# Optimization experiments

Measured on AMD Instinct MI355X. Metric: run time of the kernel, lower is better.

Reference implementation:

```python
import jax, jax.numpy as jnp
import numpy as np

T_MAX = 0.5
LN_EPS = 1e-5
B, N, D = 256, 16384, 512
NNZ = N * 33  # ~ (2*top_k+1) nonzeros per row of the sparse Laplacian
DF = 4 * D
DT = 32  # time-embedding hidden size


def _layernorm(x, g, b):
    mu = jnp.mean(x, axis=-1, keepdims=True)
    var = jnp.mean((x - mu) ** 2, axis=-1, keepdims=True)
    return (x - mu) * jax.lax.rsqrt(var + LN_EPS) * g + b


def setup_inputs() -> dict:
    key = jax.random.key(0)
    ks = jax.random.split(key, 16)

    def lin_w(k, fan_out, fan_in):
        return jax.random.normal(k, (fan_out, fan_in), jnp.float32) * (1.0 / np.sqrt(fan_in))

    inp = {}
    inp["x0"] = jax.random.uniform(ks[0], (B, N), jnp.float32)
    inp["t"] = jax.random.uniform(ks[1], (B,), jnp.float32)
    inp["L_vals"] = jax.random.normal(ks[2], (NNZ,), jnp.float32) * 0.1
    inp["W_in"] = lin_w(ks[3], D, N)
    inp["b_in"] = jnp.zeros((D,), jnp.float32)
    inp["W_out"] = lin_w(ks[4], N, D)
    inp["b_out"] = jnp.zeros((N,), jnp.float32)
    inp["W_qkv"] = lin_w(ks[5], 3 * D, D)
    inp["b_qkv"] = jnp.zeros((3 * D,), jnp.float32)
    inp["W_o"] = lin_w(ks[6], D, D)
    inp["b_o"] = jnp.zeros((D,), jnp.float32)
    inp["g1"] = jnp.ones((D,), jnp.float32)
    inp["be1"] = jnp.zeros((D,), jnp.float32)
    inp["g2"] = jnp.ones((D,), jnp.float32)
    inp["be2"] = jnp.zeros((D,), jnp.float32)
    inp["W_f1"] = lin_w(ks[7], DF, D)
    inp["b_f1"] = jnp.zeros((DF,), jnp.float32)
    inp["W_f2"] = lin_w(ks[8], D, DF)
    inp["b_f2"] = jnp.zeros((D,), jnp.float32)
    inp["W_t1"] = lin_w(ks[9], DT, 1)
    inp["b_t1"] = jnp.zeros((DT,), jnp.float32)
    inp["W_t2"] = lin_w(ks[10], D, DT)
    inp["b_t2"] = jnp.zeros((D,), jnp.float32)
    inp["L_rows"] = jax.random.randint(ks[11], (NNZ,), 0, N, jnp.int32)
    inp["L_cols"] = jax.random.randint(ks[12], (NNZ,), 0, N, jnp.int32)
    return inp


def reference(x0, t, L_vals, W_in, b_in, W_out, b_out, W_qkv, b_qkv, W_o, b_o,
              g1, be1, g2, be2, W_f1, b_f1, W_f2, b_f2, W_t1, b_t1, W_t2, b_t2,
              L_rows, L_cols):
    n_items = x0.shape[1]
    d_model = W_in.shape[0]
    t_cont = t * T_MAX  # per-sample diffusion time (explicit input, not RNG)

    # Batched sparse Laplacian diffusion (replaces the per-row torch.sparse.mm loop):
    # (L @ x.T)[i, b] = sum_e L_vals[e] * x0[b, L_cols[e]] aggregated to row L_rows[e]
    contrib = x0[:, L_cols] * L_vals                                  # (B, NNZ)
    Lx = jax.ops.segment_sum(contrib.T, L_rows, num_segments=n_items)  # (N, B)
    x_t = x0 - t_cont[:, None] * Lx.T                                  # (B, N)

    # Denoiser (eval mode: dropout off)
    h = x_t @ W_in.T + b_in                                            # (B, D)
    t_norm = t_cont / T_MAX
    te = jax.nn.silu(t_norm[:, None] @ W_t1.T + b_t1) @ W_t2.T + b_t2  # (B, D)
    h = h + te

    # MultiheadAttention on a length-1 sequence: softmax over one key is exactly 1,
    # so attn_out = out_proj(V) with V = h @ W_v.T + b_v.
    qkv = h @ W_qkv.T + b_qkv                                          # (B, 3D)
    v = qkv[:, 2 * d_model:]
    attn_out = v @ W_o.T + b_o

    h = _layernorm(h + attn_out, g1, be1)
    ff = jax.nn.gelu(h @ W_f1.T + b_f1, approximate=False) @ W_f2.T + b_f2
    h = _layernorm(h + ff, g2, be2)

    pred = h @ W_out.T + b_out                                         # (B, N)
    return jnp.mean((pred - x0) ** 2)
```

## Files before the change

kernel.cpp:

```cpp
#include <hip/hip_runtime.h>
#include <math.h>

#define Bb   256
#define Nn   16384
#define Dd   512
#define NNZn 540672
#define DFf  2048
#define SLOT 128

#define BK_BLKS 528
#define TR_BLKS 1024
#define CVT_BLKS 2048
#define MG_BLKS 64
#define BV_BLKS 2
#define BK0 0
#define TR0 (BK0 + BK_BLKS)
#define CVT0 (TR0 + TR_BLKS)
#define MG0 (CVT0 + CVT_BLKS)
#define BV0 (MG0 + MG_BLKS)
#define PREP_BLKS (BV0 + BV_BLKS)

typedef __bf16 bf16;
typedef __bf16 bf16x4 __attribute__((ext_vector_type(4)));
typedef __bf16 bf16x8 __attribute__((ext_vector_type(8)));
typedef float  f32x4  __attribute__((ext_vector_type(4)));

__device__ __forceinline__ void gload16(const void* g, void* l) {
  __builtin_amdgcn_global_load_lds(
      (const __attribute__((address_space(1))) unsigned int*)g,
      (__attribute__((address_space(3))) unsigned int*)l, 16, 0, 0);
}

__global__ __launch_bounds__(256) void k_prep(
    const float* __restrict__ w_v, const float* __restrict__ w_o,
    const float* __restrict__ w_f1, const float* __restrict__ w_f2,
    bf16* __restrict__ o_f1, bf16* __restrict__ o_f2,
    bf16* __restrict__ w_ov,
    const float* __restrict__ b_o, const float* __restrict__ b_v,
    float* __restrict__ bsum,
    const float* __restrict__ x0, bf16* __restrict__ x0T,
    const int* __restrict__ rows, const int* __restrict__ cols,
    const float* __restrict__ vals,
    int* __restrict__ counts, int2* __restrict__ ents) {
  __shared__ __align__(16) char smem[16640];
  const int blk = blockIdx.x, tid = threadIdx.x;

  if (blk < TR0) {
    int i0 = blk * 1024 + tid;
    int r[4], c[4]; float v[4];
#pragma unroll
    for (int q = 0; q < 4; q++) {
      int i = i0 + q * 256;
      r[q] = rows[i]; c[q] = cols[i]; v[q] = vals[i];
    }
    int p[4];
#pragma unroll
    for (int q = 0; q < 4; q++) p[q] = atomicAdd(&counts[r[q]], 1);
#pragma unroll
    for (int q = 0; q < 4; q++)
      if (p[q] < SLOT)
        ents[(size_t)r[q] * SLOT + p[q]] = make_int2(c[q], __float_as_int(v[q]));
  } else if (blk < CVT0) {
    float (*tile)[65] = (float(*)[65])smem;
    int bx = blk - TR0;
    int n0 = (bx & 255) * 64, b0 = (bx >> 8) * 64;
    int tx = tid & 63, ty = tid >> 6;
#pragma unroll
    for (int i = 0; i < 16; i++) {
      int bl = ty * 16 + i;
      tile[bl][tx] = x0[(size_t)(b0 + bl) * Nn + n0 + tx];
    }
    __syncthreads();
#pragma unroll
    for (int i = 0; i < 16; i++) {
      int nl = ty * 16 + i;
      x0T[(size_t)(n0 + nl) * Bb + b0 + tx] = (bf16)tile[tx][nl];
    }
  } else if (blk < MG0) {
    int v4 = (blk - CVT0) * 256 + tid;
    const float* s; bf16* d; int base;
    if (v4 < 262144) { s = w_f1; d = o_f1; base = 0; }
    else             { s = w_f2; d = o_f2; base = 262144; }
    int idx = (v4 - base) * 4;
    float4 x = *(const float4*)(s + idx);
    bf16x4 o;
    o[0] = (bf16)x.x; o[1] = (bf16)x.y; o[2] = (bf16)x.z; o[3] = (bf16)x.w;
    *(bf16x4*)(d + idx) = o;
  } else if (blk < BV0) {
    bf16* As = (bf16*)smem;
    bf16* Bs = (bf16*)(smem + 4096);
    int mg = blk - MG0;
    int m0 = (mg >> 3) * 64, n0 = (mg & 7) * 64;
    const int lane = tid & 63, w = tid >> 6;
    const int wm = w >> 1, wn = w & 1;
    f32x4 acc[2][2];
#pragma unroll
    for (int i = 0; i < 2; i++)
#pragma unroll
      for (int j = 0; j < 2; j++) acc[i][j] = {0.f, 0.f, 0.f, 0.f};
    for (int e0 = 0; e0 < Dd; e0 += 32) {
      __syncthreads();
#pragma unroll
      for (int p = 0; p < 2; p++) {
        int u = p * 256 + tid;
        int row = u >> 3, sub = u & 7;
        float4 x = *(const float4*)(w_o + (size_t)(m0 + row) * Dd + e0 + sub * 4);
        bf16x4 o;
        o[0] = (bf16)x.x; o[1] = (bf16)x.y; o[2] = (bf16)x.z; o[3] = (bf16)x.w;
        *(bf16x4*)(As + row * 32 + sub * 4) = o;
      }
#pragma unroll
      for (int p = 0; p < 2; p++) {
        int u = p * 256 + tid;
        int el = u >> 4, jq = u & 15;
        float4 x = *(const float4*)(w_v + (size_t)(e0 + el) * Dd + n0 + jq * 4);
        Bs[(jq * 4 + 0) * 32 + el] = (bf16)x.x;
        Bs[(jq * 4 + 1) * 32 + el] = (bf16)x.y;
        Bs[(jq * 4 + 2) * 32 + el] = (bf16)x.z;
        Bs[(jq * 4 + 3) * 32 + el] = (bf16)x.w;
      }
      __syncthreads();
      bf16x8 af[2], bfr[2];
#pragma unroll
      for (int i = 0; i < 2; i++)
        af[i] = *(const bf16x8*)(As + (wm * 32 + i * 16 + (lane & 15)) * 32 + (lane >> 4) * 8);
#pragma unroll
      for (int j = 0; j < 2; j++)
        bfr[j] = *(const bf16x8*)(Bs + (wn * 32 + j * 16 + (lane & 15)) * 32 + (lane >> 4) * 8);
#pragma unroll
      for (int i = 0; i < 2; i++)
#pragma unroll
        for (int j = 0; j < 2; j++)
          acc[i][j] = __builtin_amdgcn_mfma_f32_16x16x32_bf16(af[i], bfr[j], acc[i][j], 0, 0, 0);
    }
#pragma unroll
    for (int i = 0; i < 2; i++)
#pragma unroll
      for (int j = 0; j < 2; j++) {
        int jj = n0 + wn * 32 + j * 16 + (lane & 15);
        int dB = m0 + wm * 32 + i * 16 + ((lane >> 4) << 2);
#pragma unroll
        for (int r = 0; r < 4; r++)
          w_ov[(size_t)(dB + r) * Dd + jj] = (bf16)acc[i][j][r];
      }
  } else {
    int d = (blk - BV0) * 256 + tid;
    float s = b_o[d];
    for (int e = 0; e < Dd; e += 4) {
      float4 wo = *(const float4*)(w_o + (size_t)d * Dd + e);
      float4 bv = *(const float4*)(b_v + e);
      s += wo.x * bv.x + wo.y * bv.y + wo.z * bv.z + wo.w * bv.w;
    }
    bsum[d] = s;
  }
}

__global__ __launch_bounds__(256) void k_lx(const bf16x4* __restrict__ x0T4,
                                            const int* __restrict__ counts,
                                            const int2* __restrict__ ents,
                                            bf16x4* __restrict__ Lx4) {
  int w = threadIdx.x >> 6, lane = threadIdx.x & 63;
  int r = blockIdx.x * 4 + w;
  __shared__ int2 esm[4][64];
  int cnt = counts[r];
  const int2* ep = ents + (size_t)r * SLOT;
  f32x4 a = {0.f, 0.f, 0.f, 0.f}, b = {0.f, 0.f, 0.f, 0.f};
  f32x4 c = {0.f, 0.f, 0.f, 0.f}, d = {0.f, 0.f, 0.f, 0.f};
  for (int base = 0; base < cnt; base += 64) {
    int m = cnt - base; if (m > 64) m = 64;
    if (lane < m) esm[w][lane] = ep[base + lane];
    int i = 0;
    for (; i + 3 < m; i += 4) {
      int2 e0 = esm[w][i], e1 = esm[w][i + 1], e2 = esm[w][i + 2], e3 = esm[w][i + 3];
      bf16x4 x0v = x0T4[(size_t)e0.x * 64 + lane];
      bf16x4 x1v = x0T4[(size_t)e1.x * 64 + lane];
      bf16x4 x2v = x0T4[(size_t)e2.x * 64 + lane];
      bf16x4 x3v = x0T4[(size_t)e3.x * 64 + lane];
      float v0 = __int_as_float(e0.y), v1 = __int_as_float(e1.y);
      float v2 = __int_as_float(e2.y), v3 = __int_as_float(e3.y);
#pragma unroll
      for (int q = 0; q < 4; q++) {
        a[q] += v0 * (float)x0v[q];
        b[q] += v1 * (float)x1v[q];
        c[q] += v2 * (float)x2v[q];
        d[q] += v3 * (float)x3v[q];
      }
    }
    for (; i < m; i++) {
      int2 e0 = esm[w][i];
      bf16x4 x0v = x0T4[(size_t)e0.x * 64 + lane];
      float v0 = __int_as_float(e0.y);
#pragma unroll
      for (int q = 0; q < 4; q++) a[q] += v0 * (float)x0v[q];
    }
  }
  bf16x4 o;
#pragma unroll
  for (int q = 0; q < 4; q++) o[q] = (bf16)(a[q] + b[q] + c[q] + d[q]);
  Lx4[(size_t)r * 64 + lane] = o;
}

__global__ __launch_bounds__(256) void k_combine(const float* __restrict__ x0,
                                                 const bf16* __restrict__ Lx,
                                                 const float* __restrict__ t,
                                                 bf16* __restrict__ xt) {
  __shared__ float lxs[64][65];
  int n0 = blockIdx.x * 64, b0 = blockIdx.y * 64;
  int tx = threadIdx.x & 63, ty = threadIdx.x >> 6;
#pragma unroll
  for (int i = 0; i < 16; i++) {
    int nl = ty * 16 + i;
    lxs[nl][tx] = (float)Lx[(size_t)(n0 + nl) * Bb + b0 + tx];
  }
  __syncthreads();
#pragma unroll
  for (int i = 0; i < 16; i++) {
    int bl = ty * 16 + i;
    int b  = b0 + bl;
    float tc = t[b] * 0.5f;
    float v = x0[(size_t)b * Nn + n0 + tx] - tc * lxs[tx][bl];
    xt[(size_t)b * Nn + n0 + tx] = (bf16)v;
  }
}

template <int BM, int BN, int MODE, int ACT = 0, int BF32 = 0>
__global__ __launch_bounds__(256) void gemm_tn(
    const bf16* __restrict__ A, const void* __restrict__ Bmv,
    float* __restrict__ C, int N, int K, int kLen, int MN,
    const float* __restrict__ bias, const float* __restrict__ x0,
    float* __restrict__ lossOut, float* __restrict__ finalOut, int nWaves) {
  constexpr int WM = BM / 2, WN = BN / 2, FM = WM / 16, FN = WN / 16;
  constexpr int PA = (BM * 64) / 4096, PB = (BN * 64) / 4096;
  __shared__ __align__(16) bf16 As[BM * 32];
  __shared__ __align__(16) bf16 Bs[BN * 32];
  const int tid = threadIdx.x;
  const int lane = tid & 63, w = tid >> 6;
  const int wm = w >> 1, wn = w & 1;
  const int mBase = blockIdx.x * BM, nBase = blockIdx.y * BN;
  const int k0 = blockIdx.z * kLen;

  f32x4 acc[FM][FN];
#pragma unroll
  for (int i = 0; i < FM; i++)
#pragma unroll
    for (int j = 0; j < FN; j++) acc[i][j] = {0.f, 0.f, 0.f, 0.f};

  for (int kk = 0; kk < kLen; kk += 32) {
    const int k = k0 + kk;
    __syncthreads();
#pragma unroll
    for (int p = 0; p < PA; p++) {
      int u = p * 256 + tid;
      gload16(A + (size_t)(mBase + (u >> 2)) * K + k + (u & 3) * 8,
              (char*)As + p * 4096 + w * 1024);
    }
    if constexpr (BF32) {
      const float* Bf = (const float*)Bmv;
#pragma unroll
      for (int p = 0; p < BN * 32 / 1024; p++) {
        int u = p * 256 + tid;
        int row = u >> 3, sub = u & 7;
        float4 x = *(const float4*)(Bf + (size_t)(nBase + row) * K + k + sub * 4);
        bf16x4 o;
        o[0] = (bf16)x.x; o[1] = (bf16)x.y; o[2] = (bf16)x.z; o[3] = (bf16)x.w;
        *(bf16x4*)(Bs + row * 32 + sub * 4) = o;
      }
    } else {
      const bf16* Bm = (const bf16*)Bmv;
#pragma unroll
      for (int p = 0; p < PB; p++) {
        int u = p * 256 + tid;
        gload16(Bm + (size_t)(nBase + (u >> 2)) * K + k + (u & 3) * 8,
                (char*)Bs + p * 4096 + w * 1024);
      }
    }
    __syncthreads();
    bf16x8 af[FM], bfr[FN];
#pragma unroll
    for (int i = 0; i < FM; i++)
      af[i] = *(const bf16x8*)(As + (wm * WM + i * 16 + (lane & 15)) * 32 + (lane >> 4) * 8);
#pragma unroll
    for (int j = 0; j < FN; j++)
      bfr[j] = *(const bf16x8*)(Bs + (wn * WN + j * 16 + (lane & 15)) * 32 + (lane >> 4) * 8);
#pragma unroll
    for (int i = 0; i < FM; i++)
#pragma unroll
      for (int j = 0; j < FN; j++)
        acc[i][j] = __builtin_amdgcn_mfma_f32_16x16x32_bf16(af[i], bfr[j], acc[i][j], 0, 0, 0);
  }

  if constexpr (MODE == 0) {
    float* Cz = C + (size_t)blockIdx.z * MN;
#pragma unroll
    for (int i = 0; i < FM; i++)
#pragma unroll
      for (int j = 0; j < FN; j++) {
        int n  = nBase + wn * WN + j * 16 + (lane & 15);
        int mB = mBase + wm * WM + i * 16 + ((lane >> 4) << 2);
#pragma unroll
        for (int r = 0; r < 4; r++)
          Cz[(size_t)(mB + r) * N + n] = acc[i][j][r];
      }
  } else if constexpr (MODE == 1) {
    bf16* Cb = (bf16*)C;
#pragma unroll
    for (int i = 0; i < FM; i++)
#pragma unroll
      for (int j = 0; j < FN; j++) {
        int n  = nBase + wn * WN + j * 16 + (lane & 15);
        float bo = bias[n];
        int mB = mBase + wm * WM + i * 16 + ((lane >> 4) << 2);
#pragma unroll
        for (int r = 0; r < 4; r++) {
          float x = acc[i][j][r] + bo;
          if constexpr (ACT == 1)
            x = 0.5f * x * (1.f + erff(x * 0.70710678118654752f));
          Cb[(size_t)(mB + r) * N + n] = (bf16)x;
        }
      }
  } else {
    float lsum = 0.f;
#pragma unroll
    for (int i = 0; i < FM; i++)
#pragma unroll
      for (int j = 0; j < FN; j++) {
        int n  = nBase + wn * WN + j * 16 + (lane & 15);
        float bo = bias[n];
        int mB = mBase + wm * WM + i * 16 + ((lane >> 4) << 2);
#pragma unroll
        for (int r = 0; r < 4; r++) {
          float d = acc[i][j][r] + bo - x0[(size_t)(mB + r) * N + n];
          lsum += d * d;
        }
      }
    for (int off = 32; off > 0; off >>= 1) lsum += __shfl_down(lsum, off, 64);
    if (lane == 0) {
      atomicAdd(lossOut, lsum);
      __threadfence();
      unsigned prev = atomicAdd((unsigned*)(lossOut + 1), 1u);
      if ((int)prev == nWaves - 1) {
        float tot = atomicAdd(lossOut, 0.f);
        finalOut[0] = tot * (1.f / 4194304.f);
      }
    }
  }
}

template <int NS>
__global__ __launch_bounds__(512) void k_epi_h(const float* __restrict__ P,
                                               const float* __restrict__ t,
                                               const float* __restrict__ W_t1,
                                               const float* __restrict__ b_t1,
                                               const float* __restrict__ W_t2,
                                               const float* __restrict__ b_t2,
                                               const float* __restrict__ b_in,
                                               float* __restrict__ h_f32,
                                               bf16* __restrict__ h_b) {
  int b = blockIdx.x, d = threadIdx.x;
  __shared__ float s[32];
  if (d < 32) {
    float z = t[b] * W_t1[d] + b_t1[d];
    s[d] = z / (1.f + expf(-z));
  }
  __syncthreads();
  int i = b * Dd + d;
  float v = b_in[d] + b_t2[d];
#pragma unroll
  for (int sp = 0; sp < NS; sp++) v += P[sp * (Bb * Dd) + i];
#pragma unroll
  for (int j = 0; j < 32; j++) v += s[j] * W_t2[d * 32 + j];
  h_f32[i] = v;
  h_b[i] = (bf16)v;
}

template <int NS>
__global__ __launch_bounds__(512) void k_ln(const float* __restrict__ base,
                                            const float* __restrict__ add,
                                            const float* __restrict__ bias,
                                            const float* __restrict__ g,
                                            const float* __restrict__ be,
                                            float* __restrict__ out_f32,
                                            bf16* __restrict__ out_b) {
  int b = blockIdx.x, d = threadIdx.x;
  __shared__ float red[16];
  int i = b * Dd + d;
  float x = base[i] + bias[d];
#pragma unroll
  for (int sp = 0; sp < NS; sp++) x += add[sp * (Bb * Dd) + i];
  int w = d >> 6, lane = d & 63;
  float s = x;
  for (int off = 32; off > 0; off >>= 1) s += __shfl_down(s, off, 64);
  if (lane == 0) red[w] = s;
  __syncthreads();
  if (d == 0) {
    float tot = 0.f;
    for (int q = 0; q < 8; q++) tot += red[q];
    red[8] = tot * (1.f / 512.f);
  }
  __syncthreads();
  float mu = red[8];
  float c = x - mu;
  float s2 = c * c;
  for (int off = 32; off > 0; off >>= 1) s2 += __shfl_down(s2, off, 64);
  if (lane == 0) red[w] = s2;
  __syncthreads();
  if (d == 0) {
    float tot = 0.f;
    for (int q = 0; q < 8; q++) tot += red[q];
    red[8] = tot * (1.f / 512.f);
  }
  __syncthreads();
  float var = red[8];
  float y = c * rsqrtf(var + 1e-5f) * g[d] + be[d];
  if (out_f32) out_f32[i] = y;
  out_b[i] = (bf16)y;
}

extern "C" void kernel_launch(void* const* d_in, const int* in_sizes, int n_in,
                              void* d_out, int out_size, void* d_ws, size_t ws_size,
                              hipStream_t stream) {
  const float* x0    = (const float*)d_in[0];
  const float* t     = (const float*)d_in[1];
  const float* Lv    = (const float*)d_in[2];
  const float* W_in  = (const float*)d_in[3];
  const float* b_in  = (const float*)d_in[4];
  const float* W_out = (const float*)d_in[5];
  const float* b_out = (const float*)d_in[6];
  const float* W_qkv = (const float*)d_in[7];
  const float* b_qkv = (const float*)d_in[8];
  const float* W_o   = (const float*)d_in[9];
  const float* b_o   = (const float*)d_in[10];
  const float* g1    = (const float*)d_in[11];
  const float* be1   = (const float*)d_in[12];
  const float* g2    = (const float*)d_in[13];
  const float* be2   = (const float*)d_in[14];
  const float* W_f1  = (const float*)d_in[15];
  const float* b_f1  = (const float*)d_in[16];
  const float* W_f2  = (const float*)d_in[17];
  const float* b_f2  = (const float*)d_in[18];
  const float* W_t1  = (const float*)d_in[19];
  const float* b_t1  = (const float*)d_in[20];
  const float* W_t2  = (const float*)d_in[21];
  const float* b_t2  = (const float*)d_in[22];
  const int* L_rows  = (const int*)d_in[23];
  const int* L_cols  = (const int*)d_in[24];

  size_t off = 0;
  char* ws = (char*)d_ws;
  auto carve = [&](size_t bytes) -> void* {
    void* p = ws + off;
    off += (bytes + 255) & ~(size_t)255;
    return p;
  };

  bf16* W_ov_b   = (bf16*)carve((size_t)Dd * Dd * 2);
  bf16* W_f1_b   = (bf16*)carve((size_t)DFf * Dd * 2);
  bf16* W_f2_b   = (bf16*)carve((size_t)Dd * DFf * 2);
  float* bsum    = (float*)carve((size_t)Dd * 4);
  bf16* x0T_b    = (bf16*)carve((size_t)Nn * Bb * 2);
  bf16* Lx_b     = (bf16*)carve((size_t)Nn * Bb * 2);
  bf16* xt_b     = (bf16*)carve((size_t)Bb * Nn * 2);
  float* p_h     = (float*)carve((size_t)32 * Bb * Dd * 4);
  float* p_at    = (float*)carve((size_t)8 * Bb * Dd * 4);
  float* p_f2    = (float*)carve((size_t)8 * Bb * Dd * 4);
  float* h_f32   = (float*)carve((size_t)Bb * Dd * 4);
  bf16* h_b      = (bf16*)carve((size_t)Bb * Dd * 2);
  float* hln_f32 = (float*)carve((size_t)Bb * Dd * 4);
  bf16* hln_b    = (bf16*)carve((size_t)Bb * Dd * 2);
  bf16* f1_b     = (bf16*)carve((size_t)Bb * DFf * 2);
  bf16* h2_b     = (bf16*)carve((size_t)Bb * Dd * 2);
  int* counts    = (int*)carve((size_t)Nn * 4);
  float* lossw   = (float*)carve(256);
  int2* ents     = (int2*)carve((size_t)Nn * SLOT * 8);
  (void)in_sizes; (void)n_in; (void)out_size; (void)ws_size; (void)Lv;

  hipMemsetAsync(counts, 0, (size_t)Nn * 4 + 256, stream);

  k_prep<<<PREP_BLKS, 256, 0, stream>>>(
      W_qkv + (size_t)2 * Dd * Dd, W_o, W_f1, W_f2, W_f1_b, W_f2_b,
      W_ov_b, b_o, b_qkv + 2 * Dd, bsum,
      x0, x0T_b, L_rows, L_cols, Lv, counts, ents);

  k_lx<<<Nn / 4, 256, 0, stream>>>((const bf16x4*)x0T_b, counts, ents,
                                   (bf16x4*)Lx_b);
  k_combine<<<dim3(256, 4), 256, 0, stream>>>(x0, Lx_b, t, xt_b);

  gemm_tn<128, 128, 0, 0, 1><<<dim3(2, 4, 32), 256, 0, stream>>>(
      xt_b, W_in, p_h, Dd, Nn, 512, Bb * Dd, nullptr, nullptr, nullptr, nullptr, 0);
  k_epi_h<32><<<Bb, 512, 0, stream>>>(p_h, t, W_t1, b_t1, W_t2, b_t2, b_in,
                                      h_f32, h_b);

  gemm_tn<64, 64, 0><<<dim3(4, 8, 8), 256, 0, stream>>>(
      h_b, W_ov_b, p_at, Dd, Dd, 64, Bb * Dd, nullptr, nullptr, nullptr, nullptr, 0);
  k_ln<8><<<Bb, 512, 0, stream>>>(h_f32, p_at, bsum, g1, be1, hln_f32, hln_b);

  gemm_tn<64, 64, 1, 1><<<dim3(4, 32, 1), 256, 0, stream>>>(
      hln_b, W_f1_b, (float*)f1_b, DFf, Dd, 512, 0, b_f1, nullptr, nullptr, nullptr, 0);

  gemm_tn<64, 64, 0><<<dim3(4, 8, 8), 256, 0, stream>>>(
      f1_b, W_f2_b, p_f2, Dd, DFf, 256, Bb * Dd, nullptr, nullptr, nullptr, nullptr, 0);
  k_ln<8><<<Bb, 512, 0, stream>>>(hln_f32, p_f2, b_f2, g2, be2, nullptr, h2_b);

  gemm_tn<128, 128, 2, 0, 1><<<dim3(2, 128, 1), 256, 0, stream>>>(
      h2_b, W_out, nullptr, Nn, Dd, 512, 0, b_out, x0, lossw,
      (float*)d_out, 2 * 128 * 4);
}
```

Before: 338.9 us.

## Retile fp32-weight GEMMs to 256x32 and reorder prep blocks with finer scatter

Changes the big W_in and W_out GEMMs from 128x128 tiles to 256x32 tiles covering the full batch, with all four waves split along M. Each fp32 weight tile is then loaded once per block instead of being re-read by multiple M blocks, and the grid gets more blocks. The prep kernel is reordered so conversion, transpose and weight-merge blocks come first and the COO bucket scatter comes last. The scatter now handles one entry per thread instead of four. Trade-offs are a narrower N-tile per block, which may lower MFMA reuse, and changed atomic contention patterns in the scatter.

```diff
diff --git a/kernel.cpp b/kernel.cpp
--- a/kernel.cpp
+++ b/kernel.cpp
@@ -8,17 +8,17 @@
 #define DFf  2048
 #define SLOT 128
 
-#define BK_BLKS 528
-#define TR_BLKS 1024
 #define CVT_BLKS 2048
-#define MG_BLKS 64
-#define BV_BLKS 2
-#define BK0 0
-#define TR0 (BK0 + BK_BLKS)
-#define CVT0 (TR0 + TR_BLKS)
-#define MG0 (CVT0 + CVT_BLKS)
-#define BV0 (MG0 + MG_BLKS)
-#define PREP_BLKS (BV0 + BV_BLKS)
+#define TR_BLKS  1024
+#define MG_BLKS  64
+#define BV_BLKS  2
+#define BK_BLKS  2112
+#define CVT0 0
+#define TR0  (CVT0 + CVT_BLKS)
+#define MG0  (TR0 + TR_BLKS)
+#define BV0  (MG0 + MG_BLKS)
+#define BK0  (BV0 + BV_BLKS)
+#define PREP_BLKS (BK0 + BK_BLKS)
 
 typedef __bf16 bf16;
 typedef __bf16 bf16x4 __attribute__((ext_vector_type(4)));
@@ -46,38 +46,7 @@
   const int blk = blockIdx.x, tid = threadIdx.x;
 
   if (blk < TR0) {
-    int i0 = blk * 1024 + tid;
-    int r[4], c[4]; float v[4];
-#pragma unroll
-    for (int q = 0; q < 4; q++) {
-      int i = i0 + q * 256;
-      r[q] = rows[i]; c[q] = cols[i]; v[q] = vals[i];
-    }
-    int p[4];
-#pragma unroll
-    for (int q = 0; q < 4; q++) p[q] = atomicAdd(&counts[r[q]], 1);
-#pragma unroll
-    for (int q = 0; q < 4; q++)
-      if (p[q] < SLOT)
-        ents[(size_t)r[q] * SLOT + p[q]] = make_int2(c[q], __float_as_int(v[q]));
-  } else if (blk < CVT0) {
-    float (*tile)[65] = (float(*)[65])smem;
-    int bx = blk - TR0;
-    int n0 = (bx & 255) * 64, b0 = (bx >> 8) * 64;
-    int tx = tid & 63, ty = tid >> 6;
-#pragma unroll
-    for (int i = 0; i < 16; i++) {
-      int bl = ty * 16 + i;
-      tile[bl][tx] = x0[(size_t)(b0 + bl) * Nn + n0 + tx];
-    }
-    __syncthreads();
-#pragma unroll
-    for (int i = 0; i < 16; i++) {
-      int nl = ty * 16 + i;
-      x0T[(size_t)(n0 + nl) * Bb + b0 + tx] = (bf16)tile[tx][nl];
-    }
-  } else if (blk < MG0) {
-    int v4 = (blk - CVT0) * 256 + tid;
+    int v4 = blk * 256 + tid;
     const float* s; bf16* d; int base;
     if (v4 < 262144) { s = w_f1; d = o_f1; base = 0; }
     else             { s = w_f2; d = o_f2; base = 262144; }
@@ -86,6 +55,22 @@
     bf16x4 o;
     o[0] = (bf16)x.x; o[1] = (bf16)x.y; o[2] = (bf16)x.z; o[3] = (bf16)x.w;
     *(bf16x4*)(d + idx) = o;
+  } else if (blk < MG0) {
+    float (*tile)[65] = (float(*)[65])smem;
+    int bx = blk - TR0;
+    int n0 = (bx & 255) * 64, b0 = (bx >> 8) * 64;
+    int tx = tid & 63, ty = tid >> 6;
+#pragma unroll
+    for (int i = 0; i < 16; i++) {
+      int bl = ty * 16 + i;
+      tile[bl][tx] = x0[(size_t)(b0 + bl) * Nn + n0 + tx];
+    }
+    __syncthreads();
+#pragma unroll
+    for (int i = 0; i < 16; i++) {
+      int nl = ty * 16 + i;
+      x0T[(size_t)(n0 + nl) * Bb + b0 + tx] = (bf16)tile[tx][nl];
+    }
   } else if (blk < BV0) {
     bf16* As = (bf16*)smem;
     bf16* Bs = (bf16*)(smem + 4096);
@@ -143,7 +128,7 @@
         for (int r = 0; r < 4; r++)
           w_ov[(size_t)(dB + r) * Dd + jj] = (bf16)acc[i][j][r];
       }
-  } else {
+  } else if (blk < BK0) {
     int d = (blk - BV0) * 256 + tid;
     float s = b_o[d];
     for (int e = 0; e < Dd; e += 4) {
@@ -152,6 +137,12 @@
       s += wo.x * bv.x + wo.y * bv.y + wo.z * bv.z + wo.w * bv.w;
     }
     bsum[d] = s;
+  } else {
+    int i = (blk - BK0) * 256 + tid;
+    int r = rows[i];
+    int p = atomicAdd(&counts[r], 1);
+    if (p < SLOT)
+      ents[(size_t)r * SLOT + p] = make_int2(cols[i], __float_as_int(vals[i]));
   }
 }
 
@@ -223,19 +214,21 @@
   }
 }
 
-template <int BM, int BN, int MODE, int ACT = 0, int BF32 = 0>
+template <int BM, int BN, int WGM, int MODE, int ACT = 0, int BF32 = 0>
 __global__ __launch_bounds__(256) void gemm_tn(
     const bf16* __restrict__ A, const void* __restrict__ Bmv,
     float* __restrict__ C, int N, int K, int kLen, int MN,
     const float* __restrict__ bias, const float* __restrict__ x0,
     float* __restrict__ lossOut, float* __restrict__ finalOut, int nWaves) {
-  constexpr int WM = BM / 2, WN = BN / 2, FM = WM / 16, FN = WN / 16;
-  constexpr int PA = (BM * 64) / 4096, PB = (BN * 64) / 4096;
+  constexpr int WGN = 4 / WGM;
+  constexpr int WM = BM / WGM, WN = BN / WGN;
+  constexpr int FM = WM / 16, FN = WN / 16;
+  constexpr int PA = (BM * 64) / 4096, PB = BN / 64;
   __shared__ __align__(16) bf16 As[BM * 32];
   __shared__ __align__(16) bf16 Bs[BN * 32];
   const int tid = threadIdx.x;
   const int lane = tid & 63, w = tid >> 6;
-  const int wm = w >> 1, wn = w & 1;
+  const int wm = w / WGN, wn = w % WGN;
   const int mBase = blockIdx.x * BM, nBase = blockIdx.y * BN;
   const int k0 = blockIdx.z * kLen;
 
@@ -485,23 +478,23 @@
                                    (bf16x4*)Lx_b);
   k_combine<<<dim3(256, 4), 256, 0, stream>>>(x0, Lx_b, t, xt_b);
 
-  gemm_tn<128, 128, 0, 0, 1><<<dim3(2, 4, 32), 256, 0, stream>>>(
+  gemm_tn<256, 32, 4, 0, 0, 1><<<dim3(1, 16, 32), 256, 0, stream>>>(
       xt_b, W_in, p_h, Dd, Nn, 512, Bb * Dd, nullptr, nullptr, nullptr, nullptr, 0);
   k_epi_h<32><<<Bb, 512, 0, stream>>>(p_h, t, W_t1, b_t1, W_t2, b_t2, b_in,
                                       h_f32, h_b);
 
-  gemm_tn<64, 64, 0><<<dim3(4, 8, 8), 256, 0, stream>>>(
+  gemm_tn<64, 64, 2, 0><<<dim3(4, 8, 8), 256, 0, stream>>>(
       h_b, W_ov_b, p_at, Dd, Dd, 64, Bb * Dd, nullptr, nullptr, nullptr, nullptr, 0);
   k_ln<8><<<Bb, 512, 0, stream>>>(h_f32, p_at, bsum, g1, be1, hln_f32, hln_b);
 
-  gemm_tn<64, 64, 1, 1><<<dim3(4, 32, 1), 256, 0, stream>>>(
+  gemm_tn<64, 64, 2, 1, 1><<<dim3(4, 32, 1), 256, 0, stream>>>(
       hln_b, W_f1_b, (float*)f1_b, DFf, Dd, 512, 0, b_f1, nullptr, nullptr, nullptr, 0);
 
-  gemm_tn<64, 64, 0><<<dim3(4, 8, 8), 256, 0, stream>>>(
+  gemm_tn<64, 64, 2, 0><<<dim3(4, 8, 8), 256, 0, stream>>>(
       f1_b, W_f2_b, p_f2, Dd, DFf, 256, Bb * Dd, nullptr, nullptr, nullptr, nullptr, 0);
   k_ln<8><<<Bb, 512, 0, stream>>>(hln_f32, p_f2, b_f2, g2, be2, nullptr, h2_b);
 
-  gemm_tn<128, 128, 2, 0, 1><<<dim3(2, 128, 1), 256, 0, stream>>>(
+  gemm_tn<256, 32, 4, 2, 0, 1><<<dim3(1, 512, 1), 256, 0, stream>>>(
       h2_b, W_out, nullptr, Nn, Dd, 512, 0, b_out, x0, lossw,
-      (float*)d_out, 2 * 128 * 4);
-}
+      (float*)d_out, 512 * 4);
+}
```

After: 357.2 us. +5.4%, slower.
